# Kernel optimization log

Hardware: AMD Instinct MI355X
Metric: run time of the kernel (lower is better)

Reference implementation:

```python
import jax, jax.numpy as jnp
import numpy as np

B, T, D, F, E, K = 2, 2048, 1024, 4096, 8, 2

def setup_inputs() -> dict:
    key = jax.random.key(0)
    k0, k1, k2, k3 = jax.random.split(key, 4)
    return {
        "x": jax.random.normal(k0, (B, T, D), jnp.float32),
        "Wg": jax.random.normal(k1, (D, E), jnp.float32) * (D ** -0.5),
        "W1": jax.random.normal(k2, (E, D, F), jnp.float32) * (D ** -0.5),
        "b1": jnp.zeros((E, F), jnp.float32),
        "W2": jax.random.normal(k3, (E, F, D), jnp.float32) * (F ** -0.5),
        "b2": jnp.zeros((E, D), jnp.float32),
        "topk": K,
    }

def reference(x, Wg, W1, b1, W2, b2, topk):
    n_experts = Wg.shape[-1]
    # Gating logits [B, T, E]
    gating = jnp.einsum('btd,de->bte', x, Wg)
    _, idx = jax.lax.top_k(gating, topk)
    # 0/1 mask of selected experts per token [B, T, E]
    mask = jax.nn.one_hot(idx, n_experts, dtype=x.dtype).sum(axis=-2)
    # Source does `gating -= 1/mask - 1`: no-op where mask==1, -inf where mask==0
    gate = jax.nn.softmax(jnp.where(mask > 0, gating, -jnp.inf), axis=-1)
    # Dense masked per-expert compute, exactly as the source (expert(x * mask_e))
    xm = x[:, :, None, :] * mask[:, :, :, None]          # [B, T, E, D]
    h = jax.nn.gelu(jnp.einsum('bted,edf->btef', xm, W1) + b1)  # [B, T, E, F]
    out_e = jnp.einsum('btef,efd->bted', h, W2) + b2     # [B, T, E, D]
    # Gate and sum over experts
    return jnp.sum(out_e * gate[..., None], axis=-2)      # [B, T, D]
```

## Files before the change

### kernel.cpp

```cpp
#include <hip/hip_runtime.h>
#include <hip/hip_bf16.h>
#include <math.h>

#define NB 2
#define NT 2048
#define NTOK 4096
#define DD 1024
#define FF 4096
#define NE 8
#define KSEL 2
#define BM 128
#define BN 128
#define BK 64
#define ROWCAP 9216
#define ROWTILES 72
#define KP2 2

typedef __attribute__((ext_vector_type(8))) short short8_t;
typedef __attribute__((ext_vector_type(4))) float f32x4;

__device__ __forceinline__ unsigned short f2bf(float f){
  unsigned u = __float_as_uint(f);
  unsigned r = (u + 0x7fffu + ((u >> 16) & 1u)) >> 16;
  return (unsigned short)r;
}

__device__ __forceinline__ int xcd_swz(int lin, int nwg){
  int q = nwg >> 3, r = nwg & 7;
  int xcd = lin & 7, idx = lin >> 3;
  return (xcd < r ? xcd * (q + 1) : r * (q + 1) + (xcd - r) * q) + idx;
}

#define GLOAD_LDS(g, l) \
  __builtin_amdgcn_global_load_lds((const __attribute__((address_space(1))) void*)(g), \
                                   (__attribute__((address_space(3))) void*)(l), 16, 0, 0)


__global__ void k_prep(const float* __restrict__ x, const float* __restrict__ wg,
                       short* __restrict__ xb, int* __restrict__ topk_idx,
                       float* __restrict__ topk_gate, int* __restrict__ counts){
  int wid = threadIdx.x >> 6, lane = threadIdx.x & 63;
  int t = blockIdx.x * 4 + wid;
  const float* xr = x + (size_t)t * DD;
  short* xbr = xb + (size_t)t * DD;
  double acc[NE];
#pragma unroll
  for (int e = 0; e < NE; ++e) acc[e] = 0.0;
#pragma unroll
  for (int p = 0; p < 4; ++p){
    int d = p * 256 + lane * 4;
    float4 v = *(const float4*)(xr + d);
    short4 o;
    o.x = (short)f2bf(v.x); o.y = (short)f2bf(v.y);
    o.z = (short)f2bf(v.z); o.w = (short)f2bf(v.w);
    *(short4*)(xbr + d) = o;
    const float* w0 = wg + (size_t)d * NE;
    float vv[4] = {v.x, v.y, v.z, v.w};
#pragma unroll
    for (int j = 0; j < 4; ++j){
      double xv = (double)vv[j];
#pragma unroll
      for (int e = 0; e < NE; ++e) acc[e] += xv * (double)w0[j * NE + e];
    }
  }
#pragma unroll
  for (int e = 0; e < NE; ++e){
#pragma unroll
    for (int s = 32; s; s >>= 1) acc[e] += __shfl_xor(acc[e], s, 64);
  }
  if (lane == 0){
    int i0 = 0; double v0 = acc[0];
#pragma unroll
    for (int e = 1; e < NE; ++e) if (acc[e] > v0){ v0 = acc[e]; i0 = e; }
    int i1 = -1; double v1 = -1e300;
#pragma unroll
    for (int e = 0; e < NE; ++e) if (e != i0 && acc[e] > v1){ v1 = acc[e]; i1 = e; }
    double g0 = 1.0 / (1.0 + exp(v1 - v0));
    topk_idx[2 * t] = i0; topk_idx[2 * t + 1] = i1;
    topk_gate[2 * t] = (float)g0; topk_gate[2 * t + 1] = (float)(1.0 - g0);
    atomicAdd(&counts[i0], 1);
    atomicAdd(&counts[i1], 1);
  }
}


__global__ void k_transpose_all(const float* __restrict__ W1, const float* __restrict__ W2,
                                short* __restrict__ w1t, short* __restrict__ w2t){
  __shared__ short T[64][132];
  int id = blockIdx.x;
  bool isW2 = id >= 4096;
  int rem = id & 4095;
  int e = rem >> 9;
  int tr = rem & 511;
  int R, C, c0, r0;
  const float* in; short* out;
  if (!isW2){ R = DD; C = FF; c0 = (tr & 63) * 64; r0 = (tr >> 6) * 128;
              in = W1 + (size_t)e * R * C; out = w1t + (size_t)e * R * C; }
  else      { R = FF; C = DD; c0 = (tr & 15) * 64; r0 = (tr >> 4) * 128;
              in = W2 + (size_t)e * R * C; out = w2t + (size_t)e * R * C; }
  int t = threadIdx.x;
  int rr = t >> 4, c4 = (t & 15) * 4;
#pragma unroll
  for (int p = 0; p < 8; ++p){
    int row = p * 16 + rr;
    float4 v = *(const float4*)(in + (size_t)(r0 + row) * C + c0 + c4);
    T[c4 + 0][row] = (short)f2bf(v.x);
    T[c4 + 1][row] = (short)f2bf(v.y);
    T[c4 + 2][row] = (short)f2bf(v.z);
    T[c4 + 3][row] = (short)f2bf(v.w);
  }
  __syncthreads();
  int c8 = (t & 15) * 8;
#pragma unroll
  for (int q = 0; q < 4; ++q){
    int orow = q * 16 + rr;
    short4 lo = *(const short4*)&T[orow][c8];
    short4 hi = *(const short4*)&T[orow][c8 + 4];
    short8_t w;
    w[0] = lo.x; w[1] = lo.y; w[2] = lo.z; w[3] = lo.w;
    w[4] = hi.x; w[5] = hi.y; w[6] = hi.z; w[7] = hi.w;
    *(short8_t*)(out + (size_t)(c0 + orow) * R + r0 + c8) = w;
  }
}


__global__ void k_route_all(const int* __restrict__ counts, const int* __restrict__ topk_idx,
                            const float* __restrict__ topk_gate, int* __restrict__ poff_g,
                            int* __restrict__ row_token, float* __restrict__ row_gate,
                            int* __restrict__ slot_of){
  __shared__ int poff[NE + 1], cur[NE], rends[NE];
  if (threadIdx.x == 0){
    int off = 0;
    for (int e = 0; e < NE; ++e){
      poff[e] = off; cur[e] = off; rends[e] = off + counts[e];
      off += (counts[e] + BM - 1) & ~(BM - 1);
    }
    poff[NE] = off;
    for (int e = 0; e <= NE; ++e) poff_g[e] = poff[e];
  }
  __syncthreads();
  for (int t = threadIdx.x; t < NTOK; t += 256){
#pragma unroll
    for (int k = 0; k < KSEL; ++k){
      int e = topk_idx[2 * t + k];
      float g = topk_gate[2 * t + k];
      int slot = atomicAdd(&cur[e], 1);
      row_token[slot] = t;
      row_gate[slot] = g;
      slot_of[2 * t + k] = slot;
    }
  }
  __syncthreads();
#pragma unroll
  for (int e = 0; e < NE; ++e)
    for (int s = rends[e] + (int)threadIdx.x; s < poff[e + 1]; s += 256){
      row_token[s] = 0; row_gate[s] = 0.f;
    }
}


__launch_bounds__(256, 4)
__global__ void k_gemm1(const short* __restrict__ xb, const short* __restrict__ w1t,
                        const float* __restrict__ b1, short* __restrict__ h,
                        const int* __restrict__ row_token, const int* __restrict__ poff){
  __shared__ short As[BM * BK];
  __shared__ short Bs[BN * BK];
  int lin = blockIdx.x + ROWTILES * blockIdx.y;
  int wg = xcd_swz(lin, ROWTILES * (FF / BN));
  int bx = wg >> 5, by = wg & 31;
  int row0 = bx * BM;
  if (row0 >= poff[NE]) return;
  int e = 0;
  while (row0 >= poff[e + 1]) ++e;
  int n0 = by * BN;
  int tid = threadIdx.x;

  const short* asrc[4]; const short* bsrc[4];
#pragma unroll
  for (int p = 0; p < 4; ++p){
    int L = p * 256 + tid;
    int r = L >> 3, cs = L & 7;
    int cd = cs ^ (r & 7);
    int tok = row_token[row0 + r];
    asrc[p] = xb + (size_t)tok * DD + cd * 8;
    bsrc[p] = w1t + (size_t)e * FF * DD + (size_t)(n0 + r) * DD + cd * 8;
  }
  short* alds = As + tid * 8;
  short* blds = Bs + tid * 8;

  f32x4 acc[4][4];
#pragma unroll
  for (int i = 0; i < 4; ++i)
#pragma unroll
    for (int j = 0; j < 4; ++j) acc[i][j] = (f32x4){0.f, 0.f, 0.f, 0.f};

  int wid = tid >> 6, lane = tid & 63;
  int wr = wid >> 1, wc = wid & 1;
  int lrow = lane & 15, lk = lane >> 4;

  for (int k0 = 0; k0 < DD; k0 += BK){
#pragma unroll
    for (int p = 0; p < 4; ++p){
      GLOAD_LDS(asrc[p] + k0, alds + p * 2048);
      GLOAD_LDS(bsrc[p] + k0, blds + p * 2048);
    }
    __syncthreads();
#pragma unroll
    for (int kk = 0; kk < 2; ++kk){
      short8_t a[4], b[4];
      int c = kk * 4 + lk;
#pragma unroll
      for (int m = 0; m < 4; ++m){
        int r = wr * 64 + m * 16 + lrow;
        a[m] = *(const short8_t*)(As + r * BK + ((c ^ (r & 7)) * 8));
      }
#pragma unroll
      for (int n = 0; n < 4; ++n){
        int r = wc * 64 + n * 16 + lrow;
        b[n] = *(const short8_t*)(Bs + r * BK + ((c ^ (r & 7)) * 8));
      }
#pragma unroll
      for (int m = 0; m < 4; ++m)
#pragma unroll
        for (int n = 0; n < 4; ++n)
          acc[m][n] = __builtin_amdgcn_mfma_f32_16x16x32_bf16(a[m], b[n], acc[m][n], 0, 0, 0);
    }
    __syncthreads();
  }

  const float* b1e = b1 + (size_t)e * FF;
#pragma unroll
  for (int n = 0; n < 4; ++n){
    int col = n0 + wc * 64 + n * 16 + lrow;
    float bias = b1e[col];
#pragma unroll
    for (int m = 0; m < 4; ++m){
#pragma unroll
      for (int j = 0; j < 4; ++j){
        int row = row0 + wr * 64 + m * 16 + lk * 4 + j;
        float v = acc[m][n][j] + bias;
        float u = 0.7978845608028654f * (v + 0.044715f * v * v * v);
        float g = v / (1.0f + __expf(-2.0f * u));
        h[(size_t)row * FF + col] = (short)f2bf(g);
      }
    }
  }
}


__launch_bounds__(256, 4)
__global__ void k_gemm2(const short* __restrict__ h, const short* __restrict__ w2t,
                        const float* __restrict__ b2, float* __restrict__ ya,
                        float* __restrict__ yb, const int* __restrict__ poff){
  __shared__ short As[BM * BK];
  __shared__ short Bs[BN * BK];
  int lin = blockIdx.x + ROWTILES * (blockIdx.y + (DD / BN) * blockIdx.z);
  int wg = xcd_swz(lin, ROWTILES * (DD / BN) * KP2);
  int by = wg & 7, bx = (wg >> 3) % ROWTILES, kz = (wg >> 3) / ROWTILES;
  int row0 = bx * BM;
  if (row0 >= poff[NE]) return;
  int e = 0;
  while (row0 >= poff[e + 1]) ++e;
  int n0 = by * BN;
  int tid = threadIdx.x;

  const short* asrc[4]; const short* bsrc[4];
#pragma unroll
  for (int p = 0; p < 4; ++p){
    int L = p * 256 + tid;
    int r = L >> 3, cs = L & 7;
    int cd = cs ^ (r & 7);
    asrc[p] = h + (size_t)(row0 + r) * FF + cd * 8;
    bsrc[p] = w2t + (size_t)e * DD * FF + (size_t)(n0 + r) * FF + cd * 8;
  }
  short* alds = As + tid * 8;
  short* blds = Bs + tid * 8;

  f32x4 acc[4][4];
#pragma unroll
  for (int i = 0; i < 4; ++i)
#pragma unroll
    for (int j = 0; j < 4; ++j) acc[i][j] = (f32x4){0.f, 0.f, 0.f, 0.f};

  int wid = tid >> 6, lane = tid & 63;
  int wr = wid >> 1, wc = wid & 1;
  int lrow = lane & 15, lk = lane >> 4;

  int kbeg = kz * (FF / KP2), kend = kbeg + FF / KP2;
  for (int k0 = kbeg; k0 < kend; k0 += BK){
#pragma unroll
    for (int p = 0; p < 4; ++p){
      GLOAD_LDS(asrc[p] + k0, alds + p * 2048);
      GLOAD_LDS(bsrc[p] + k0, blds + p * 2048);
    }
    __syncthreads();
#pragma unroll
    for (int kk = 0; kk < 2; ++kk){
      short8_t a[4], b[4];
      int c = kk * 4 + lk;
#pragma unroll
      for (int m = 0; m < 4; ++m){
        int r = wr * 64 + m * 16 + lrow;
        a[m] = *(const short8_t*)(As + r * BK + ((c ^ (r & 7)) * 8));
      }
#pragma unroll
      for (int n = 0; n < 4; ++n){
        int r = wc * 64 + n * 16 + lrow;
        b[n] = *(const short8_t*)(Bs + r * BK + ((c ^ (r & 7)) * 8));
      }
#pragma unroll
      for (int m = 0; m < 4; ++m)
#pragma unroll
        for (int n = 0; n < 4; ++n)
          acc[m][n] = __builtin_amdgcn_mfma_f32_16x16x32_bf16(a[m], b[n], acc[m][n], 0, 0, 0);
    }
    __syncthreads();
  }

  float* y = (kz == 0) ? ya : yb;
  const float* b2e = b2 + (size_t)e * DD;
#pragma unroll
  for (int n = 0; n < 4; ++n){
    int col = n0 + wc * 64 + n * 16 + lrow;
    float bias = (kz == 0) ? b2e[col] : 0.0f;
#pragma unroll
    for (int m = 0; m < 4; ++m){
#pragma unroll
      for (int j = 0; j < 4; ++j){
        int row = row0 + wr * 64 + m * 16 + lk * 4 + j;
        y[(size_t)row * DD + col] = acc[m][n][j] + bias;
      }
    }
  }
}


__global__ void k_combine(const float* __restrict__ ya, const float* __restrict__ yb,
                          const int* __restrict__ slot_of, const float* __restrict__ topk_gate,
                          float* __restrict__ out){
  int i = blockIdx.x * 256 + threadIdx.x;
  int t = i >> 8;
  int c4 = (i & 255) * 4;
  int s0 = slot_of[2 * t], s1 = slot_of[2 * t + 1];
  float g0 = topk_gate[2 * t], g1 = topk_gate[2 * t + 1];
  float4 a0 = *(const float4*)(ya + (size_t)s0 * DD + c4);
  float4 b0 = *(const float4*)(yb + (size_t)s0 * DD + c4);
  float4 a1 = *(const float4*)(ya + (size_t)s1 * DD + c4);
  float4 b1 = *(const float4*)(yb + (size_t)s1 * DD + c4);
  float4 o;
  o.x = g0 * (a0.x + b0.x) + g1 * (a1.x + b1.x);
  o.y = g0 * (a0.y + b0.y) + g1 * (a1.y + b1.y);
  o.z = g0 * (a0.z + b0.z) + g1 * (a1.z + b1.z);
  o.w = g0 * (a0.w + b0.w) + g1 * (a1.w + b1.w);
  *(float4*)(out + (size_t)t * DD + c4) = o;
}


extern "C" void kernel_launch(void* const* d_in, const int* in_sizes, int n_in,
                              void* d_out, int out_size, void* d_ws, size_t ws_size,
                              hipStream_t stream){
  (void)in_sizes; (void)n_in; (void)out_size; (void)ws_size;
  const float* x  = (const float*)d_in[0];
  const float* Wg = (const float*)d_in[1];
  const float* W1 = (const float*)d_in[2];
  const float* b1 = (const float*)d_in[3];
  const float* W2 = (const float*)d_in[4];
  const float* b2 = (const float*)d_in[5];
  float* out = (float*)d_out;
  char* ws = (char*)d_ws;

  int*   counts    = (int*)(ws + 0);
  int*   poff      = (int*)(ws + 256);
  int*   topk_idx  = (int*)(ws + 1024);
  float* topk_gate = (float*)(ws + 33792);
  int*   row_token = (int*)(ws + 66560);
  float* row_gate  = (float*)(ws + 103424);
  int*   slot_of   = (int*)(ws + 140288);
  short* xb        = (short*)(ws + 173056);
  short* w1t       = (short*)(ws + 8561664);
  short* w2t       = (short*)(ws + 75670528);
  short* h         = (short*)(ws + 142779392);
  float* ya        = (float*)(ws + 173056);
  float* yb        = (float*)(ws + 37921792);

  hipMemsetAsync(counts, 0, 32, stream);

  k_prep<<<dim3(NTOK / 4), 256, 0, stream>>>(x, Wg, xb, topk_idx, topk_gate, counts);
  k_transpose_all<<<dim3(8192), 256, 0, stream>>>(W1, W2, w1t, w2t);
  k_route_all<<<dim3(1), 256, 0, stream>>>(counts, topk_idx, topk_gate, poff,
                                           row_token, row_gate, slot_of);
  k_gemm1<<<dim3(ROWTILES, FF / BN), 256, 0, stream>>>(xb, w1t, b1, h, row_token, poff);
  k_gemm2<<<dim3(ROWTILES, DD / BN, KP2), 256, 0, stream>>>(h, w2t, b2, ya, yb, poff);
  k_combine<<<dim3(NTOK * DD / 4 / 256), 256, 0, stream>>>(ya, yb, slot_of, topk_gate, out);
}
```

Baseline: 473.9 us.

## Double-buffer LDS in expert GEMMs and group tiles for L2 reuse

Both expert GEMM kernels now use two LDS buffers, so the global-to-LDS load of the next K tile is issued before the MFMA work on the current tile, leaving one barrier per iteration instead of two. The launch grids become 1D, and the tile index is remapped into 8x8 (gemm1) and 4x8 (gemm2) supertile groups to improve L2 reuse of weight and activation tiles. The point is to hide global load latency behind compute. In exchange, LDS use doubles and the occupancy hint drops from 4 to 2 blocks per CU.

```diff
diff --git a/kernel.cpp b/kernel.cpp
--- a/kernel.cpp
+++ b/kernel.cpp
@@ -159,15 +159,16 @@
 }
 
 
-__launch_bounds__(256, 4)
+__launch_bounds__(256, 2)
 __global__ void k_gemm1(const short* __restrict__ xb, const short* __restrict__ w1t,
                         const float* __restrict__ b1, short* __restrict__ h,
                         const int* __restrict__ row_token, const int* __restrict__ poff){
-  __shared__ short As[BM * BK];
-  __shared__ short Bs[BN * BK];
-  int lin = blockIdx.x + ROWTILES * blockIdx.y;
-  int wg = xcd_swz(lin, ROWTILES * (FF / BN));
-  int bx = wg >> 5, by = wg & 31;
+  __shared__ short As[2][BM * BK];
+  __shared__ short Bs[2][BN * BK];
+  int wg = xcd_swz(blockIdx.x, ROWTILES * (FF / BN));
+  int g = wg >> 6, t6 = wg & 63;
+  int bx = (g >> 2) * 8 + (t6 & 7);
+  int by = (g & 3) * 8 + (t6 >> 3);
   int row0 = bx * BM;
   if (row0 >= poff[NE]) return;
   int e = 0;
@@ -185,8 +186,6 @@
     asrc[p] = xb + (size_t)tok * DD + cd * 8;
     bsrc[p] = w1t + (size_t)e * FF * DD + (size_t)(n0 + r) * DD + cd * 8;
   }
-  short* alds = As + tid * 8;
-  short* blds = Bs + tid * 8;
 
   f32x4 acc[4][4];
 #pragma unroll
@@ -198,13 +197,26 @@
   int wr = wid >> 1, wc = wid & 1;
   int lrow = lane & 15, lk = lane >> 4;
 
-  for (int k0 = 0; k0 < DD; k0 += BK){
-#pragma unroll
-    for (int p = 0; p < 4; ++p){
-      GLOAD_LDS(asrc[p] + k0, alds + p * 2048);
-      GLOAD_LDS(bsrc[p] + k0, blds + p * 2048);
-    }
-    __syncthreads();
+#pragma unroll
+  for (int p = 0; p < 4; ++p){
+    GLOAD_LDS(asrc[p], &As[0][0] + tid * 8 + p * 2048);
+    GLOAD_LDS(bsrc[p], &Bs[0][0] + tid * 8 + p * 2048);
+  }
+  asm volatile("s_waitcnt vmcnt(0)" ::: "memory");
+  __builtin_amdgcn_s_barrier();
+
+  const int NTILE = DD / BK;
+#pragma unroll 2
+  for (int kt = 0; kt < NTILE; ++kt){
+    int cur = kt & 1;
+    if (kt + 1 < NTILE){
+      int k0 = (kt + 1) * BK;
+#pragma unroll
+      for (int p = 0; p < 4; ++p){
+        GLOAD_LDS(asrc[p] + k0, &As[cur ^ 1][0] + tid * 8 + p * 2048);
+        GLOAD_LDS(bsrc[p] + k0, &Bs[cur ^ 1][0] + tid * 8 + p * 2048);
+      }
+    }
 #pragma unroll
     for (int kk = 0; kk < 2; ++kk){
       short8_t a[4], b[4];
@@ -212,12 +224,12 @@
 #pragma unroll
       for (int m = 0; m < 4; ++m){
         int r = wr * 64 + m * 16 + lrow;
-        a[m] = *(const short8_t*)(As + r * BK + ((c ^ (r & 7)) * 8));
+        a[m] = *(const short8_t*)(&As[cur][0] + r * BK + ((c ^ (r & 7)) * 8));
       }
 #pragma unroll
       for (int n = 0; n < 4; ++n){
         int r = wc * 64 + n * 16 + lrow;
-        b[n] = *(const short8_t*)(Bs + r * BK + ((c ^ (r & 7)) * 8));
+        b[n] = *(const short8_t*)(&Bs[cur][0] + r * BK + ((c ^ (r & 7)) * 8));
       }
 #pragma unroll
       for (int m = 0; m < 4; ++m)
@@ -225,38 +237,46 @@
         for (int n = 0; n < 4; ++n)
           acc[m][n] = __builtin_amdgcn_mfma_f32_16x16x32_bf16(a[m], b[n], acc[m][n], 0, 0, 0);
     }
-    __syncthreads();
+    if (kt + 1 < NTILE){
+      asm volatile("s_waitcnt vmcnt(0)" ::: "memory");
+      __builtin_amdgcn_s_barrier();
+    }
   }
 
   const float* b1e = b1 + (size_t)e * FF;
-#pragma unroll
-  for (int n = 0; n < 4; ++n){
-    int col = n0 + wc * 64 + n * 16 + lrow;
-    float bias = b1e[col];
-#pragma unroll
-    for (int m = 0; m < 4; ++m){
-#pragma unroll
-      for (int j = 0; j < 4; ++j){
-        int row = row0 + wr * 64 + m * 16 + lk * 4 + j;
-        float v = acc[m][n][j] + bias;
+  float bias[4];
+#pragma unroll
+  for (int n = 0; n < 4; ++n) bias[n] = b1e[n0 + wc * 64 + n * 16 + lrow];
+#pragma unroll
+  for (int m = 0; m < 4; ++m){
+#pragma unroll
+    for (int j = 0; j < 4; ++j){
+      int row = row0 + wr * 64 + m * 16 + lk * 4 + j;
+      short* hr = h + (size_t)row * FF + n0 + wc * 64 + lrow;
+#pragma unroll
+      for (int n = 0; n < 4; ++n){
+        float v = acc[m][n][j] + bias[n];
         float u = 0.7978845608028654f * (v + 0.044715f * v * v * v);
-        float g = v / (1.0f + __expf(-2.0f * u));
-        h[(size_t)row * FF + col] = (short)f2bf(g);
-      }
-    }
-  }
-}
-
-
-__launch_bounds__(256, 4)
+        float gl = v / (1.0f + __expf(-2.0f * u));
+        hr[n * 16] = (short)f2bf(gl);
+      }
+    }
+  }
+}
+
+
+__launch_bounds__(256, 2)
 __global__ void k_gemm2(const short* __restrict__ h, const short* __restrict__ w2t,
                         const float* __restrict__ b2, float* __restrict__ ya,
                         float* __restrict__ yb, const int* __restrict__ poff){
-  __shared__ short As[BM * BK];
-  __shared__ short Bs[BN * BK];
-  int lin = blockIdx.x + ROWTILES * (blockIdx.y + (DD / BN) * blockIdx.z);
-  int wg = xcd_swz(lin, ROWTILES * (DD / BN) * KP2);
-  int by = wg & 7, bx = (wg >> 3) % ROWTILES, kz = (wg >> 3) / ROWTILES;
+  __shared__ short As[2][BM * BK];
+  __shared__ short Bs[2][BN * BK];
+  int wg = xcd_swz(blockIdx.x, ROWTILES * (DD / BN) * KP2);
+  int kz = wg / (ROWTILES * (DD / BN));
+  int c5 = wg % (ROWTILES * (DD / BN));
+  int g = c5 >> 5, t5 = c5 & 31;
+  int bx = g * 4 + (t5 & 3);
+  int by = t5 >> 2;
   int row0 = bx * BM;
   if (row0 >= poff[NE]) return;
   int e = 0;
@@ -273,8 +293,6 @@
     asrc[p] = h + (size_t)(row0 + r) * FF + cd * 8;
     bsrc[p] = w2t + (size_t)e * DD * FF + (size_t)(n0 + r) * FF + cd * 8;
   }
-  short* alds = As + tid * 8;
-  short* blds = Bs + tid * 8;
 
   f32x4 acc[4][4];
 #pragma unroll
@@ -286,14 +304,27 @@
   int wr = wid >> 1, wc = wid & 1;
   int lrow = lane & 15, lk = lane >> 4;
 
-  int kbeg = kz * (FF / KP2), kend = kbeg + FF / KP2;
-  for (int k0 = kbeg; k0 < kend; k0 += BK){
-#pragma unroll
-    for (int p = 0; p < 4; ++p){
-      GLOAD_LDS(asrc[p] + k0, alds + p * 2048);
-      GLOAD_LDS(bsrc[p] + k0, blds + p * 2048);
-    }
-    __syncthreads();
+  int kbeg = kz * (FF / KP2);
+#pragma unroll
+  for (int p = 0; p < 4; ++p){
+    GLOAD_LDS(asrc[p] + kbeg, &As[0][0] + tid * 8 + p * 2048);
+    GLOAD_LDS(bsrc[p] + kbeg, &Bs[0][0] + tid * 8 + p * 2048);
+  }
+  asm volatile("s_waitcnt vmcnt(0)" ::: "memory");
+  __builtin_amdgcn_s_barrier();
+
+  const int NTILE = (FF / KP2) / BK;
+#pragma unroll 2
+  for (int kt = 0; kt < NTILE; ++kt){
+    int cur = kt & 1;
+    if (kt + 1 < NTILE){
+      int k0 = kbeg + (kt + 1) * BK;
+#pragma unroll
+      for (int p = 0; p < 4; ++p){
+        GLOAD_LDS(asrc[p] + k0, &As[cur ^ 1][0] + tid * 8 + p * 2048);
+        GLOAD_LDS(bsrc[p] + k0, &Bs[cur ^ 1][0] + tid * 8 + p * 2048);
+      }
+    }
 #pragma unroll
     for (int kk = 0; kk < 2; ++kk){
       short8_t a[4], b[4];
@@ -301,12 +332,12 @@
 #pragma unroll
       for (int m = 0; m < 4; ++m){
         int r = wr * 64 + m * 16 + lrow;
-        a[m] = *(const short8_t*)(As + r * BK + ((c ^ (r & 7)) * 8));
+        a[m] = *(const short8_t*)(&As[cur][0] + r * BK + ((c ^ (r & 7)) * 8));
       }
 #pragma unroll
       for (int n = 0; n < 4; ++n){
         int r = wc * 64 + n * 16 + lrow;
-        b[n] = *(const short8_t*)(Bs + r * BK + ((c ^ (r & 7)) * 8));
+        b[n] = *(const short8_t*)(&Bs[cur][0] + r * BK + ((c ^ (r & 7)) * 8));
       }
 #pragma unroll
       for (int m = 0; m < 4; ++m)
@@ -314,7 +345,10 @@
         for (int n = 0; n < 4; ++n)
           acc[m][n] = __builtin_amdgcn_mfma_f32_16x16x32_bf16(a[m], b[n], acc[m][n], 0, 0, 0);
     }
-    __syncthreads();
+    if (kt + 1 < NTILE){
+      asm volatile("s_waitcnt vmcnt(0)" ::: "memory");
+      __builtin_amdgcn_s_barrier();
+    }
   }
 
   float* y = (kz == 0) ? ya : yb;
@@ -389,7 +423,7 @@
   k_transpose_all<<<dim3(8192), 256, 0, stream>>>(W1, W2, w1t, w2t);
   k_route_all<<<dim3(1), 256, 0, stream>>>(counts, topk_idx, topk_gate, poff,
                                            row_token, row_gate, slot_of);
-  k_gemm1<<<dim3(ROWTILES, FF / BN), 256, 0, stream>>>(xb, w1t, b1, h, row_token, poff);
-  k_gemm2<<<dim3(ROWTILES, DD / BN, KP2), 256, 0, stream>>>(h, w2t, b2, ya, yb, poff);
+  k_gemm1<<<dim3(ROWTILES * (FF / BN)), 256, 0, stream>>>(xb, w1t, b1, h, row_token, poff);
+  k_gemm2<<<dim3(ROWTILES * (DD / BN) * KP2), 256, 0, stream>>>(h, w2t, b2, ya, yb, poff);
   k_combine<<<dim3(NTOK * DD / 4 / 256), 256, 0, stream>>>(ya, yb, slot_of, topk_gate, out);
 }
```

New measurement: 501.8 us. 5.9% more time.
